# Kernel tuning notes

Hardware: AMD Instinct MI355X
Metric: run time of the kernel (lower is better)

The kernel has to match this reference:

```python
import jax, jax.numpy as jnp
import numpy as np
from functools import partial

G, N, E = 512, 256, 1024
F_IN, EMB, H, NCLS = 30, 256, 3, 2
NEG_SLOPE = 0.2
K1 = int(np.ceil(0.8 * N))   # 205
K2 = int(np.ceil(0.8 * K1))  # 164
K3 = int(np.ceil(0.8 * K2))  # 132


def _gat(x, src, dst, emask, W, asrc, adst, b):
    # Single-graph GATConv (PyG semantics, eval mode): x [n,f], edges [e] + validity mask.
    # Adds self-loops (PyG default), edge-softmax grouped by destination node.
    n = x.shape[0]
    h = (x @ W.T).reshape(n, H, EMB)                      # [n,H,C]
    a_s = (h * asrc).sum(-1)                              # [n,H]
    a_d = (h * adst).sum(-1)                              # [n,H]
    loops = jnp.arange(n, dtype=src.dtype)
    s = jnp.concatenate([src, loops])
    d = jnp.concatenate([dst, loops])
    m = jnp.concatenate([emask, jnp.ones((n,), bool)])
    logit = jax.nn.leaky_relu(a_s[s] + a_d[d], NEG_SLOPE)  # [e+n,H]
    logit = jnp.where(m[:, None], logit, -1e9)
    mx = jax.ops.segment_max(logit, d, num_segments=n)     # stable softmax per dst
    w = jnp.exp(logit - mx[d]) * m[:, None]
    den = jax.ops.segment_sum(w, d, num_segments=n)
    alpha = w / den[d]
    out = jax.ops.segment_sum(alpha[:, :, None] * h[s], d, num_segments=n)  # [n,H,C]
    return out.reshape(n, H * EMB) + b


def _pool(x, src, dst, emask, p, k):
    # TopKPooling: score = tanh((x.p)/||p||); keep top-k nodes, scale by score,
    # remap edge indices and invalidate edges touching dropped nodes.
    n = x.shape[0]
    score = jnp.tanh((x @ p) / jnp.linalg.norm(p))
    vals, perm = jax.lax.top_k(score, k)
    xn = x[perm] * vals[:, None]
    inv = jnp.full((n,), -1, jnp.int32).at[perm].set(jnp.arange(k, dtype=jnp.int32))
    ns, nd = inv[src], inv[dst]
    nm = emask & (ns >= 0) & (nd >= 0)
    return xn, jnp.maximum(ns, 0), jnp.maximum(nd, 0), nm


_gat_b = jax.vmap(_gat, in_axes=(0, 0, 0, 0, None, None, None, None))


def _pool_b(x, src, dst, m, p, k):
    return jax.vmap(partial(_pool, k=k), in_axes=(0, 0, 0, 0, None))(x, src, dst, m, p)


def _readout(x):
    # global_max_pool || global_mean_pool per graph: [G,n,d] -> [G,2d]
    return jnp.concatenate([x.max(axis=1), x.mean(axis=1)], axis=-1)


def _forward(x, edge_src, edge_dst, params):
    (W1, as1, ad1, b1, ht1w, ht1b, p1,
     W2, as2, ad2, b2, ht2w, ht2b, p2,
     W3, as3, ad3, b3, ht3w, ht3b, p3,
     l1w, l1b, l2w, l2b) = params
    src, dst = edge_src, edge_dst
    m = jnp.ones(src.shape, bool)
    h = _gat_b(x, src, dst, m, W1, as1, ad1, b1) @ ht1w.T + ht1b
    h, src, dst, m = _pool_b(h, src, dst, m, p1, K1)
    x1 = _readout(h)
    h = _gat_b(h, src, dst, m, W2, as2, ad2, b2) @ ht2w.T + ht2b
    h, src, dst, m = _pool_b(h, src, dst, m, p2, K2)
    x2 = _readout(h)
    h = _gat_b(h, src, dst, m, W3, as3, ad3, b3) @ ht3w.T + ht3b
    h, src, dst, m = _pool_b(h, src, dst, m, p3, K3)
    x3 = _readout(h)
    z = x1 + x2 + x3
    z = jax.nn.relu(z @ l1w.T + l1b)  # F.dropout is a no-op in eval mode
    return z @ l2w.T + l2b


def setup_inputs() -> dict:
    key = jax.random.key(0)
    keys = iter(jax.random.split(key, 64))
    def nrm(shape, s=0.05):
        return jax.random.normal(next(keys), shape, jnp.float32) * s
    inp = {
        "x": jax.random.normal(next(keys), (G, N, F_IN), jnp.float32),
        "edge_src": jax.random.randint(next(keys), (G, E), 0, N, jnp.int32),
        "edge_dst": jax.random.randint(next(keys), (G, E), 0, N, jnp.int32),
    }
    for i, fin in ((1, F_IN), (2, EMB), (3, EMB)):
        inp[f"W{i}"] = nrm((H * EMB, fin))
        inp[f"asrc{i}"] = nrm((H, EMB))
        inp[f"adst{i}"] = nrm((H, EMB))
        inp[f"b{i}"] = jnp.zeros((H * EMB,), jnp.float32)
        inp[f"ht{i}_w"] = nrm((EMB, H * EMB))
        inp[f"ht{i}_b"] = jnp.zeros((EMB,), jnp.float32)
        inp[f"p{i}"] = nrm((EMB,), 1.0)
    inp["lin1_w"] = nrm((EMB, 2 * EMB))
    inp["lin1_b"] = jnp.zeros((EMB,), jnp.float32)
    inp["lin2_w"] = nrm((NCLS, EMB))
    inp["lin2_b"] = jnp.zeros((NCLS,), jnp.float32)
    return inp


def reference(x, edge_src, edge_dst,
              W1, asrc1, adst1, b1, ht1_w, ht1_b, p1,
              W2, asrc2, adst2, b2, ht2_w, ht2_b, p2,
              W3, asrc3, adst3, b3, ht3_w, ht3_b, p3,
              lin1_w, lin1_b, lin2_w, lin2_b):
    params = (W1, asrc1, adst1, b1, ht1_w, ht1_b, p1,
              W2, asrc2, adst2, b2, ht2_w, ht2_b, p2,
              W3, asrc3, adst3, b3, ht3_w, ht3_b, p3,
              lin1_w, lin1_b, lin2_w, lin2_b)
    return _forward(x, edge_src, edge_dst, params)
```

## Files before the change

kernel.cpp:

```cpp
#include <hip/hip_runtime.h>
#include <hip/hip_bf16.h>

#define GG 512
#define NMAX 256
#define EE 1024
#define HH 3
#define EMB 256
#define NEDGE 1280
#define NEG 0.2f

typedef __attribute__((ext_vector_type(8))) short bf16x8;
typedef __attribute__((ext_vector_type(4))) float f32x4;
#define MFMA16(A,B,C) __builtin_amdgcn_mfma_f32_16x16x32_bf16((A),(B),(C),0,0,0)

__device__ inline void bsplit(float v, unsigned short& s0, unsigned short& s1,
                              unsigned short& s2) {
  __hip_bfloat16 b0 = __float2bfloat16(v);
  float r1 = v - __bfloat162float(b0);
  __hip_bfloat16 b1 = __float2bfloat16(r1);
  float r2 = r1 - __bfloat162float(b1);
  __hip_bfloat16 b2 = __float2bfloat16(r2);
  s0 = *(unsigned short*)&b0; s1 = *(unsigned short*)&b1; s2 = *(unsigned short*)&b2;
}

__global__ void k_prep_wa(const float* __restrict__ W, const float* __restrict__ asrc,
                          const float* __restrict__ adst, float* __restrict__ wa_s,
                          float* __restrict__ wa_d, int f) {
  int t = blockIdx.x * blockDim.x + threadIdx.x;
  int tot = HH * f;
  if (t >= 2 * tot) return;
  int which = t / tot;
  int r = t - which * tot;
  int hd = r / f, ff = r - hd * f;
  const float* a = which ? adst : asrc;
  float s = 0.f;
  for (int c = 0; c < EMB; ++c)
    s += a[hd * EMB + c] * W[(size_t)(hd * EMB + c) * f + ff];
  (which ? wa_d : wa_s)[r] = s;
}

__global__ void k_prep_mcatP(const float* __restrict__ W, const float* __restrict__ htw,
                             float* __restrict__ mcat, int f, int KP) {
  int t = blockIdx.x * blockDim.x + threadIdx.x;
  if (t >= KP * EMB) return;
  int row = t >> 8, j = t & 255;
  float s = 0.f;
  if (row < 3 * f) {
    int hd = row / f, ff = row - hd * f;
    for (int c = 0; c < EMB; ++c)
      s += htw[(size_t)j * (HH * EMB) + hd * EMB + c] * W[(size_t)(hd * EMB + c) * f + ff];
  }
  mcat[(size_t)row * EMB + j] = s;
}

__global__ void k_prep_bt3(const float* __restrict__ mcat, unsigned short* __restrict__ B0,
                           unsigned short* __restrict__ B1, unsigned short* __restrict__ B2,
                           int KP) {
  int t = blockIdx.x * blockDim.x + threadIdx.x;
  if (t >= 256 * KP) return;
  int n = t / KP, k = t - n * KP;
  float v = mcat[(size_t)k * 256 + n];
  unsigned short s0, s1, s2;
  bsplit(v, s0, s1, s2);
  B0[t] = s0; B1[t] = s1; B2[t] = s2;
}

__global__ void k_prep_bb(const float* __restrict__ b, const float* __restrict__ htw,
                          const float* __restrict__ htb, float* __restrict__ bb) {
  int j = threadIdx.x;
  float s = htb[j];
  for (int k = 0; k < HH * EMB; ++k) s += b[k] * htw[(size_t)j * (HH * EMB) + k];
  bb[j] = s;
}

__global__ void k_prep_q(const float* __restrict__ mcat, const float* __restrict__ p,
                         double* __restrict__ qv, int f) {
  int r = blockIdx.x * blockDim.x + threadIdx.x;
  if (r >= 3 * f) return;
  double s = 0.0;
  for (int c = 0; c < EMB; ++c) s += (double)mcat[(size_t)r * EMB + c] * (double)p[c];
  qv[r] = s;
}

__global__ void k_prep_sc(const float* __restrict__ p, const float* __restrict__ bb,
                          double* __restrict__ sc2) {
  __shared__ double sh[256], sh2[256];
  int t = threadIdx.x;
  double pv = (double)p[t];
  sh[t] = pv * pv;
  sh2[t] = (double)bb[t] * pv;
  __syncthreads();
  for (int s = 128; s > 0; s >>= 1) {
    if (t < s) { sh[t] += sh[t + s]; sh2[t] += sh2[t + s]; }
    __syncthreads();
  }
  if (t == 0) { sc2[0] = sh2[0]; sc2[1] = sqrt(sh[0]); }
}

__global__ void k_initedges(const int* __restrict__ s_in, const int* __restrict__ d_in_,
                            int* __restrict__ es, int* __restrict__ ed,
                            int* __restrict__ em, int gc) {
  int t = blockIdx.x * blockDim.x + threadIdx.x;
  if (t >= gc * EE) return;
  es[t] = s_in[t]; ed[t] = d_in_[t]; em[t] = 1;
}

__global__ __launch_bounds__(256) void k_attn2(
    const float* __restrict__ x, const float* __restrict__ wa_s,
    const float* __restrict__ wa_d, const double* __restrict__ qv,
    float* __restrict__ a_s, float* __restrict__ a_d, double* __restrict__ tdot,
    int gc, int n_in, int f) {
  int t = blockIdx.x * blockDim.x + threadIdx.x;
  if (t >= gc * n_in) return;
  int g = t / n_in, i = t - g * n_in;
  const float* xr = x + ((size_t)g * n_in + i) * f;
  float s0 = 0, s1 = 0, s2 = 0, d0 = 0, d1 = 0, d2 = 0;
  double t0 = 0, t1 = 0, t2 = 0;
  for (int c = 0; c < f; ++c) {
    float xv = xr[c];
    s0 += xv * wa_s[0 * f + c]; s1 += xv * wa_s[1 * f + c]; s2 += xv * wa_s[2 * f + c];
    d0 += xv * wa_d[0 * f + c]; d1 += xv * wa_d[1 * f + c]; d2 += xv * wa_d[2 * f + c];
    double xd = (double)xv;
    t0 += xd * qv[0 * f + c]; t1 += xd * qv[1 * f + c]; t2 += xd * qv[2 * f + c];
  }
  size_t o = ((size_t)g * NMAX + i) * HH;
  a_s[o + 0] = s0; a_s[o + 1] = s1; a_s[o + 2] = s2;
  a_d[o + 0] = d0; a_d[o + 1] = d1; a_d[o + 2] = d2;
  tdot[o + 0] = t0; tdot[o + 1] = t1; tdot[o + 2] = t2;
}

__global__ __launch_bounds__(256) void k_graph(
    int* __restrict__ es, int* __restrict__ ed, int* __restrict__ em,
    const float* __restrict__ a_s, const float* __restrict__ a_d,
    const double* __restrict__ tdot, const double* __restrict__ sc2,
    float4* __restrict__ a4, int* __restrict__ coff, int* __restrict__ elist,
    int* __restrict__ sel, float* __restrict__ val, int n_in, int kout) {
  __shared__ float lgs[NEDGE * 3];
  __shared__ unsigned short sdst[NEDGE], ssrc[NEDGE];
  __shared__ unsigned char sval[NEDGE];
  __shared__ int cnt2[256];
  __shared__ int off[257];
  __shared__ int elist_s[NEDGE];
  __shared__ float sscore[256];
  __shared__ unsigned long long keys[256];
  __shared__ int inv[256];
  int g = blockIdx.x, tid = threadIdx.x;
  int etot = EE + n_in;
  cnt2[tid] = 0;
  __syncthreads();
  for (int e = tid; e < etot; e += 256) {
    int s, d, v;
    if (e < EE) { s = es[g * EE + e]; d = ed[g * EE + e]; v = em[g * EE + e]; }
    else { s = d = e - EE; v = 1; }
    sdst[e] = (unsigned short)d; ssrc[e] = (unsigned short)s; sval[e] = (unsigned char)v;
    if (v) {
      const float* as = a_s + ((size_t)g * NMAX + s) * HH;
      const float* ad = a_d + ((size_t)g * NMAX + d) * HH;
#pragma unroll
      for (int h = 0; h < HH; ++h) {
        float lv = as[h] + ad[h];
        lgs[e * 3 + h] = lv > 0.f ? lv : NEG * lv;
      }
      atomicAdd(&cnt2[d], 1);
    }
  }
  __syncthreads();
  if (tid == 0) {
    int run = 0;
    for (int i = 0; i < n_in; ++i) { int c = cnt2[i]; off[i] = run; run += c; }
    off[n_in] = run;
  }
  __syncthreads();
  for (int i = tid; i <= n_in; i += 256) coff[g * 257 + i] = off[i];
  cnt2[tid] = 0;
  __syncthreads();
  for (int e = tid; e < etot; e += 256) {
    if (sval[e]) {
      int d = sdst[e];
      int pos = atomicAdd(&cnt2[d], 1);
      elist_s[off[d] + pos] = e;
    }
  }
  __syncthreads();
  if (tid < n_in) {
    int o0 = off[tid], o1 = off[tid + 1];
    for (int i = o0 + 1; i < o1; ++i) {
      int key = elist_s[i];
      int j = i - 1;
      while (j >= o0 && elist_s[j] > key) { elist_s[j + 1] = elist_s[j]; --j; }
      elist_s[j + 1] = key;
    }
    for (int q = o0; q < o1; ++q) elist[g * NEDGE + q] = elist_s[q];
  }
  __syncthreads();
  float sc = -3e38f;
  if (tid < n_in) {
    int o0 = off[tid], o1 = off[tid + 1];
    float m0 = -1e30f, m1 = -1e30f, m2 = -1e30f;
    for (int q = o0; q < o1; ++q) {
      int e = elist_s[q];
      m0 = fmaxf(m0, lgs[e * 3 + 0]);
      m1 = fmaxf(m1, lgs[e * 3 + 1]);
      m2 = fmaxf(m2, lgs[e * 3 + 2]);
    }
    float d0 = 0, d1 = 0, d2 = 0;
    for (int q = o0; q < o1; ++q) {
      int e = elist_s[q];
      d0 += expf(lgs[e * 3 + 0] - m0);
      d1 += expf(lgs[e * 3 + 1] - m1);
      d2 += expf(lgs[e * 3 + 2] - m2);
    }
    float r0 = 1.f / d0, r1 = 1.f / d1, r2 = 1.f / d2;
    double s = 0.0;
    for (int q = o0; q < o1; ++q) {
      int e = elist_s[q];
      float w0 = expf(lgs[e * 3 + 0] - m0) * r0;
      float w1 = expf(lgs[e * 3 + 1] - m1) * r1;
      float w2 = expf(lgs[e * 3 + 2] - m2) * r2;
      int src = ssrc[e];
      float4 av; av.x = w0; av.y = w1; av.z = w2; av.w = __int_as_float(src);
      a4[(size_t)g * NEDGE + e] = av;
      const double* td = tdot + ((size_t)g * NMAX + src) * HH;
      s += (double)w0 * td[0] + (double)w1 * td[1] + (double)w2 * td[2];
    }
    sc = (float)tanh((s + sc2[0]) / sc2[1]);
  }
  sscore[tid] = sc;
  unsigned int u = __float_as_uint(sc);
  unsigned int ord = (u & 0x80000000u) ? ~u : (u | 0x80000000u);
  unsigned long long key = ((unsigned long long)(~ord) << 32) | (unsigned int)tid;
  if (tid >= n_in) key = 0xFFFFFFFF00000000ull | (unsigned int)tid;
  keys[tid] = key;
  __syncthreads();
  for (int kk = 2; kk <= 256; kk <<= 1) {
    for (int j = kk >> 1; j > 0; j >>= 1) {
      int ixj = tid ^ j;
      if (ixj > tid) {
        unsigned long long a = keys[tid], b = keys[ixj];
        bool up = ((tid & kk) == 0);
        if (up ? (a > b) : (a < b)) { keys[tid] = b; keys[ixj] = a; }
      }
      __syncthreads();
    }
  }
  inv[tid] = -1;
  __syncthreads();
  if (tid < kout) {
    int pi = (int)(keys[tid] & 0xFFFFu);
    inv[pi] = tid;
    sel[g * 256 + tid] = pi;
    val[g * 256 + tid] = sscore[pi];
  }
  __syncthreads();
  for (int e = tid; e < EE; e += 256) {
    int s = es[g * EE + e], d = ed[g * EE + e], m = em[g * EE + e];
    int ns = inv[s], nd = inv[d];
    int nm = (m && ns >= 0 && nd >= 0) ? 1 : 0;
    es[g * EE + e] = ns < 0 ? 0 : ns;
    ed[g * EE + e] = nd < 0 ? 0 : nd;
    em[g * EE + e] = nm;
  }
}

template<bool F256>
__global__ __launch_bounds__(256) void k_gather_sel(
    const float* __restrict__ xin, const float4* __restrict__ a4,
    const int* __restrict__ coff, const int* __restrict__ elist,
    const int* __restrict__ sel,
    unsigned short* __restrict__ A0, unsigned short* __restrict__ A1,
    unsigned short* __restrict__ A2,
    int gc, int n_in, int n_out, int f, int KP) {
  int wid = (blockIdx.x * blockDim.x + threadIdx.x) >> 6;
  int lane = threadIdx.x & 63;
  if (wid >= gc * n_out) return;
  int g = wid / n_out, j = wid - g * n_out;
  int pi = sel[(g << 8) + j];
  int o0 = coff[g * 257 + pi], o1 = coff[g * 257 + pi + 1];
  const float* xg = xin + (size_t)g * n_in * f;
  size_t rb = ((size_t)g * n_out + j) * (size_t)KP;
  if (F256) {
    float4 acc0 = make_float4(0, 0, 0, 0);
    float4 acc1 = make_float4(0, 0, 0, 0);
    float4 acc2 = make_float4(0, 0, 0, 0);
    for (int t = o0; t < o1; ++t) {
      int e = elist[g * NEDGE + t];
      float4 a = a4[(size_t)g * NEDGE + e];
      int src = __float_as_int(a.w);
      float4 xv = ((const float4*)(xg + (size_t)src * 256))[lane];
      acc0.x += a.x * xv.x; acc0.y += a.x * xv.y; acc0.z += a.x * xv.z; acc0.w += a.x * xv.w;
      acc1.x += a.y * xv.x; acc1.y += a.y * xv.y; acc1.z += a.y * xv.z; acc1.w += a.y * xv.w;
      acc2.x += a.z * xv.x; acc2.y += a.z * xv.y; acc2.z += a.z * xv.z; acc2.w += a.z * xv.w;
    }
    float4 accs[3] = {acc0, acc1, acc2};
#pragma unroll
    for (int h = 0; h < 3; ++h) {
      size_t idx = rb + (size_t)h * 256 + lane * 4;
      ushort4 u0, u1, u2;
      bsplit(accs[h].x, u0.x, u1.x, u2.x);
      bsplit(accs[h].y, u0.y, u1.y, u2.y);
      bsplit(accs[h].z, u0.z, u1.z, u2.z);
      bsplit(accs[h].w, u0.w, u1.w, u2.w);
      *(ushort4*)&A0[idx] = u0;
      *(ushort4*)&A1[idx] = u1;
      *(ushort4*)&A2[idx] = u2;
    }
  } else {
    for (int kk = lane; kk < 96; kk += 64) {
      float v = 0.f;
      if (kk < 90) {
        int h = kk / 30, cc = kk - h * 30;
        for (int t = o0; t < o1; ++t) {
          int e = elist[g * NEDGE + t];
          float4 a = a4[(size_t)g * NEDGE + e];
          int src = __float_as_int(a.w);
          float al = (h == 0) ? a.x : ((h == 1) ? a.y : a.z);
          v += al * xg[(size_t)src * 30 + cc];
        }
      }
      unsigned short s0, s1, s2;
      bsplit(v, s0, s1, s2);
      A0[rb + kk] = s0; A1[rb + kk] = s1; A2[rb + kk] = s2;
    }
  }
}

__global__ __launch_bounds__(256) void k_mgemm(
    const unsigned short* __restrict__ A0, const unsigned short* __restrict__ A1,
    const unsigned short* __restrict__ A2,
    const unsigned short* __restrict__ B0, const unsigned short* __restrict__ B1,
    const unsigned short* __restrict__ B2,
    const float* __restrict__ bias, const float* __restrict__ val,
    float* __restrict__ xout, int Mrows, int KP, int n_out, int nbx) {
  __shared__ unsigned short As[3][64 * 32];
  __shared__ unsigned short Bs[3][64 * 32];
  int tid = threadIdx.x;
  int jj = blockIdx.x & 31;
  int rr0 = (blockIdx.x >> 5) * 8 + (jj & 7);
  int cc0 = jj >> 3;
  if (rr0 >= nbx) return;
  int row0 = rr0 * 64;
  int col0 = cc0 * 64;
  int lane = tid & 63, w = tid >> 6;
  int kg = lane >> 4, r16 = lane & 15;
  int wr = (w >> 1) * 32, wc = (w & 1) * 32;
  int sr = tid >> 2, sj = tid & 3;
  int sp = sj ^ ((sr >> 1) & 3);
  const unsigned short* Ap[3] = {A0, A1, A2};
  const unsigned short* Bp[3] = {B0, B1, B2};

  f32x4 acc[2][2];
#pragma unroll
  for (int i = 0; i < 2; ++i)
#pragma unroll
    for (int j = 0; j < 2; ++j) acc[i][j] = (f32x4){0.f, 0.f, 0.f, 0.f};

  int nkt = KP >> 5;
  for (int kt = 0; kt < nkt; ++kt) {
    int k0 = kt << 5;
    int gra = row0 + sr;
    int grb = col0 + sr;
#pragma unroll
    for (int p = 0; p < 3; ++p) {
      uint4 va = make_uint4(0, 0, 0, 0);
      if (gra < Mrows) va = *(const uint4*)&Ap[p][(size_t)gra * KP + k0 + (sj << 3)];
      *(uint4*)&As[p][sr * 32 + (sp << 3)] = va;
      uint4 vb = *(const uint4*)&Bp[p][(size_t)grb * KP + k0 + (sj << 3)];
      *(uint4*)&Bs[p][sr * 32 + (sp << 3)] = vb;
    }
    __syncthreads();
    bf16x8 af[2][3], bf[2][3];
#pragma unroll
    for (int fm = 0; fm < 2; ++fm) {
      int row = wr + (fm << 4) + r16;
      int pk = kg ^ ((row >> 1) & 3);
#pragma unroll
      for (int p = 0; p < 3; ++p)
        af[fm][p] = *(const bf16x8*)&As[p][row * 32 + (pk << 3)];
    }
#pragma unroll
    for (int fn = 0; fn < 2; ++fn) {
      int col = wc + (fn << 4) + r16;
      int pk = kg ^ ((col >> 1) & 3);
#pragma unroll
      for (int p = 0; p < 3; ++p)
        bf[fn][p] = *(const bf16x8*)&Bs[p][col * 32 + (pk << 3)];
    }
#pragma unroll
    for (int fm = 0; fm < 2; ++fm)
#pragma unroll
      for (int fn = 0; fn < 2; ++fn) {
        f32x4 c = acc[fm][fn];
        c = MFMA16(af[fm][0], bf[fn][0], c);
        c = MFMA16(af[fm][0], bf[fn][1], c);
        c = MFMA16(af[fm][1], bf[fn][0], c);
        c = MFMA16(af[fm][0], bf[fn][2], c);
        c = MFMA16(af[fm][2], bf[fn][0], c);
        c = MFMA16(af[fm][1], bf[fn][1], c);
        acc[fm][fn] = c;
      }
    __syncthreads();
  }
#pragma unroll
  for (int fm = 0; fm < 2; ++fm)
#pragma unroll
    for (int fn = 0; fn < 2; ++fn) {
      int colg = col0 + wc + (fn << 4) + r16;
      float bi = bias[colg];
#pragma unroll
      for (int rr = 0; rr < 4; ++rr) {
        int rowg = row0 + wr + (fm << 4) + (kg << 2) + rr;
        if (rowg < Mrows) {
          int gg = rowg / n_out, j = rowg - gg * n_out;
          xout[((size_t)gg * n_out + j) * EMB + colg] =
              (acc[fm][fn][rr] + bi) * val[(gg << 8) + j];
        }
      }
    }
}

__global__ void k_readout(const float* __restrict__ x, float* __restrict__ z,
                          int n_out, int g0) {
  int g = blockIdx.x, c = threadIdx.x;
  float mx = -3e38f, sm = 0.f;
  for (int j = 0; j < n_out; ++j) {
    float v = x[((size_t)g * n_out + j) * EMB + c];
    mx = fmaxf(mx, v);
    sm += v;
  }
  z[(size_t)(g0 + g) * 512 + c] += mx;
  z[(size_t)(g0 + g) * 512 + 256 + c] += sm / (float)n_out;
}

__global__ void k_mlp(const float* __restrict__ z, const float* __restrict__ l1w,
                      const float* __restrict__ l1b, const float* __restrict__ l2w,
                      const float* __restrict__ l2b, float* __restrict__ out) {
  __shared__ float zs[512];
  __shared__ float h1[256];
  int g = blockIdx.x, tid = threadIdx.x;
  zs[tid] = z[(size_t)g * 512 + tid];
  zs[256 + tid] = z[(size_t)g * 512 + 256 + tid];
  __syncthreads();
  float s = l1b[tid];
  for (int c = 0; c < 512; ++c) s += zs[c] * l1w[(size_t)tid * 512 + c];
  h1[tid] = s > 0.f ? s : 0.f;
  __syncthreads();
  if (tid < 2) {
    float o = l2b[tid];
    for (int c = 0; c < 256; ++c) o += h1[c] * l2w[(size_t)tid * 256 + c];
    out[g * 2 + tid] = o;
  }
}

extern "C" void kernel_launch(void* const* d_in, const int* in_sizes, int n_in_cnt,
                              void* d_out, int out_size, void* d_ws, size_t ws_size,
                              hipStream_t stream) {
  (void)in_sizes; (void)n_in_cnt; (void)out_size;
  const float* x0 = (const float*)d_in[0];
  const int* e_src = (const int*)d_in[1];
  const int* e_dst = (const int*)d_in[2];
  struct LP { const float *W, *as, *ad, *b, *hw, *hb, *p; int f, nin, nout, KP; };
  LP L[3];
  for (int l = 0; l < 3; ++l) {
    int base = 3 + l * 7;
    L[l].W  = (const float*)d_in[base + 0];
    L[l].as = (const float*)d_in[base + 1];
    L[l].ad = (const float*)d_in[base + 2];
    L[l].b  = (const float*)d_in[base + 3];
    L[l].hw = (const float*)d_in[base + 4];
    L[l].hb = (const float*)d_in[base + 5];
    L[l].p  = (const float*)d_in[base + 6];
  }
  L[0].f = 30;  L[1].f = 256; L[2].f = 256;
  L[0].nin = 256; L[0].nout = 205; L[0].KP = 96;
  L[1].nin = 205; L[1].nout = 164; L[1].KP = 768;
  L[2].nin = 164; L[2].nout = 132; L[2].KP = 768;
  const float* l1w = (const float*)d_in[24];
  const float* l1b = (const float*)d_in[25];
  const float* l2w = (const float*)d_in[26];
  const float* l2b = (const float*)d_in[27];
  float* out = (float*)d_out;

  char* w = (char*)d_ws;
  char* wend = w + ws_size;
  auto alloc = [&](size_t bytes) {
    char* r = w; w += (bytes + 255) & ~(size_t)255; return r;
  };
  float*  z = (float*)alloc((size_t)GG * 512 * 4);
  float *wa_s[3], *wa_d[3], *mcatP[3], *bbv[3];
  unsigned short *bt0[3], *bt1[3], *bt2[3];
  double *qv[3], *sc2[3];
  for (int l = 0; l < 3; ++l) {
    int KP = (l == 0) ? 96 : 768;
    wa_s[l]  = (float*)alloc((size_t)HH * 256 * 4);
    wa_d[l]  = (float*)alloc((size_t)HH * 256 * 4);
    mcatP[l] = (float*)alloc((size_t)768 * EMB * 4);
    bbv[l]   = (float*)alloc((size_t)EMB * 4);
    bt0[l]   = (unsigned short*)alloc((size_t)256 * KP * 2);
    bt1[l]   = (unsigned short*)alloc((size_t)256 * KP * 2);
    bt2[l]   = (unsigned short*)alloc((size_t)256 * KP * 2);
    qv[l]    = (double*)alloc((size_t)768 * 8);
    sc2[l]   = (double*)alloc(256);
  }

  const size_t AMAX = (size_t)164 * 768;
  const size_t APAD = (size_t)64 * 768;
  size_t fixed_used = (size_t)(w - (char*)d_ws);
  size_t per_g = (size_t)205 * EMB * 4
               + AMAX * 2 * 3
               + (size_t)NMAX * HH * 4 * 2
               + (size_t)NMAX * HH * 8
               + (size_t)NEDGE * 16
               + (size_t)EE * 4 * 3
               + (size_t)257 * 4 + (size_t)NEDGE * 4
               + (size_t)256 * 4 * 2
               + 24 * 256;
  size_t avail = (ws_size > fixed_used + 1048576) ? (ws_size - fixed_used - 1048576) : 0;
  int Gc = (int)(avail / per_g);
  if (Gc > GG) Gc = GG;
  if (Gc < 1) Gc = 1;
  int nchunks = (GG + Gc - 1) / Gc;
  Gc = (GG + nchunks - 1) / nchunks;

  float*  xbuf = (float*)alloc((size_t)Gc * 205 * EMB * 4);
  unsigned short* AP0 = (unsigned short*)alloc(((size_t)Gc * AMAX + APAD) * 2);
  unsigned short* AP1 = (unsigned short*)alloc(((size_t)Gc * AMAX + APAD) * 2);
  unsigned short* AP2 = (unsigned short*)alloc(((size_t)Gc * AMAX + APAD) * 2);
  float*  a_s  = (float*)alloc((size_t)Gc * NMAX * HH * 4);
  float*  a_d  = (float*)alloc((size_t)Gc * NMAX * HH * 4);
  double* tdot = (double*)alloc((size_t)Gc * NMAX * HH * 8);
  float4* a4   = (float4*)alloc((size_t)Gc * NEDGE * 16);
  int*    es   = (int*)alloc((size_t)Gc * EE * 4);
  int*    ed   = (int*)alloc((size_t)Gc * EE * 4);
  int*    em   = (int*)alloc((size_t)Gc * EE * 4);
  int*    coff = (int*)alloc((size_t)Gc * 257 * 4);
  int*    elist= (int*)alloc((size_t)Gc * NEDGE * 4);
  int*    sel  = (int*)alloc((size_t)Gc * 256 * 4);
  float*  val  = (float*)alloc((size_t)Gc * 256 * 4);
  if (w > wend) return;

  (void)hipMemsetAsync(z, 0, (size_t)GG * 512 * 4, stream);

  for (int l = 0; l < 3; ++l) {
    int f = L[l].f, KP = L[l].KP;
    k_prep_wa<<<(2 * HH * f + 255) / 256, 256, 0, stream>>>(L[l].W, L[l].as, L[l].ad, wa_s[l], wa_d[l], f);
    k_prep_mcatP<<<(KP * EMB + 255) / 256, 256, 0, stream>>>(L[l].W, L[l].hw, mcatP[l], f, KP);
    k_prep_bt3<<<(256 * KP + 255) / 256, 256, 0, stream>>>(mcatP[l], bt0[l], bt1[l], bt2[l], KP);
    k_prep_bb<<<1, 256, 0, stream>>>(L[l].b, L[l].hw, L[l].hb, bbv[l]);
    k_prep_q<<<(3 * f + 255) / 256, 256, 0, stream>>>(mcatP[l], L[l].p, qv[l], f);
    k_prep_sc<<<1, 256, 0, stream>>>(L[l].p, bbv[l], sc2[l]);
  }

  for (int g0 = 0; g0 < GG; g0 += Gc) {
    int gc = (GG - g0 < Gc) ? (GG - g0) : Gc;
    { int tot = gc * EE;
      k_initedges<<<(tot + 255) / 256, 256, 0, stream>>>(
          e_src + (size_t)g0 * EE, e_dst + (size_t)g0 * EE, es, ed, em, gc); }
    const float* xin = x0 + (size_t)g0 * 256 * 30;
    for (int l = 0; l < 3; ++l) {
      int f = L[l].f, nin = L[l].nin, nout = L[l].nout, KP = L[l].KP;
      k_attn2<<<(gc * nin + 255) / 256, 256, 0, stream>>>(xin, wa_s[l], wa_d[l], qv[l], a_s, a_d, tdot, gc, nin, f);
      k_graph<<<gc, 256, 0, stream>>>(es, ed, em, a_s, a_d, tdot, sc2[l], a4, coff, elist, sel, val, nin, nout);
      { int waves = gc * nout;
        if (f == 256)
          k_gather_sel<true><<<(waves * 64 + 255) / 256, 256, 0, stream>>>(
              xin, a4, coff, elist, sel, AP0, AP1, AP2, gc, nin, nout, f, KP);
        else
          k_gather_sel<false><<<(waves * 64 + 255) / 256, 256, 0, stream>>>(
              xin, a4, coff, elist, sel, AP0, AP1, AP2, gc, nin, nout, f, KP);
      }
      { int Mrows = gc * nout;
        int nbx = (Mrows + 63) / 64;
        int nblk = ((nbx + 7) / 8) * 32;
        k_mgemm<<<nblk, 256, 0, stream>>>(AP0, AP1, AP2, bt0[l], bt1[l], bt2[l],
                                          bbv[l], val, xbuf, Mrows, KP, nout, nbx);
      }
      k_readout<<<gc, 256, 0, stream>>>(xbuf, z, nout, g0);
      xin = xbuf;
    }
  }
  k_mlp<<<GG, 256, 0, stream>>>(z, l1w, l1b, l2w, l2b, out);
}
```

Measured before the change: 2.163 ms.

## Double-buffer GEMM LDS tiles and fold edge init into graph kernel

The split-bf16 MFMA GEMM now double-buffers its A/B shared-memory tiles. The next K-tile's global loads are issued into registers before computing the current tile, which removes one barrier per iteration and overlaps memory latency with MFMA work. Launch bounds ask for 3 blocks per SM, and doubling the LDS footprint may limit occupancy. Separately, the edge-init kernel is removed: the first layer's graph kernel reads the input edges directly, and edge remapping reuses the indices already cached in shared memory instead of reloading them from global.

```diff
diff --git a/kernel.cpp b/kernel.cpp
--- a/kernel.cpp
+++ b/kernel.cpp
@@ -95,14 +95,6 @@
     __syncthreads();
   }
   if (t == 0) { sc2[0] = sh2[0]; sc2[1] = sqrt(sh[0]); }
-}
-
-__global__ void k_initedges(const int* __restrict__ s_in, const int* __restrict__ d_in_,
-                            int* __restrict__ es, int* __restrict__ ed,
-                            int* __restrict__ em, int gc) {
-  int t = blockIdx.x * blockDim.x + threadIdx.x;
-  if (t >= gc * EE) return;
-  es[t] = s_in[t]; ed[t] = d_in_[t]; em[t] = 1;
 }
 
 __global__ __launch_bounds__(256) void k_attn2(
@@ -130,6 +122,7 @@
 }
 
 __global__ __launch_bounds__(256) void k_graph(
+    const int* __restrict__ src_in, const int* __restrict__ dst_in, int first,
     int* __restrict__ es, int* __restrict__ ed, int* __restrict__ em,
     const float* __restrict__ a_s, const float* __restrict__ a_d,
     const double* __restrict__ tdot, const double* __restrict__ sc2,
@@ -150,8 +143,10 @@
   __syncthreads();
   for (int e = tid; e < etot; e += 256) {
     int s, d, v;
-    if (e < EE) { s = es[g * EE + e]; d = ed[g * EE + e]; v = em[g * EE + e]; }
-    else { s = d = e - EE; v = 1; }
+    if (e < EE) {
+      if (first) { s = src_in[g * EE + e]; d = dst_in[g * EE + e]; v = 1; }
+      else { s = es[g * EE + e]; d = ed[g * EE + e]; v = em[g * EE + e]; }
+    } else { s = d = e - EE; v = 1; }
     sdst[e] = (unsigned short)d; ssrc[e] = (unsigned short)s; sval[e] = (unsigned char)v;
     if (v) {
       const float* as = a_s + ((size_t)g * NMAX + s) * HH;
@@ -253,7 +248,7 @@
   }
   __syncthreads();
   for (int e = tid; e < EE; e += 256) {
-    int s = es[g * EE + e], d = ed[g * EE + e], m = em[g * EE + e];
+    int s = ssrc[e], d = sdst[e], m = sval[e];
     int ns = inv[s], nd = inv[d];
     int nm = (m && ns >= 0 && nd >= 0) ? 1 : 0;
     es[g * EE + e] = ns < 0 ? 0 : ns;
@@ -324,15 +319,15 @@
   }
 }
 
-__global__ __launch_bounds__(256) void k_mgemm(
+__global__ __launch_bounds__(256, 3) void k_mgemm(
     const unsigned short* __restrict__ A0, const unsigned short* __restrict__ A1,
     const unsigned short* __restrict__ A2,
     const unsigned short* __restrict__ B0, const unsigned short* __restrict__ B1,
     const unsigned short* __restrict__ B2,
     const float* __restrict__ bias, const float* __restrict__ val,
     float* __restrict__ xout, int Mrows, int KP, int n_out, int nbx) {
-  __shared__ unsigned short As[3][64 * 32];
-  __shared__ unsigned short Bs[3][64 * 32];
+  __shared__ unsigned short As[2][3][64 * 32];
+  __shared__ unsigned short Bs[2][3][64 * 32];
   int tid = threadIdx.x;
   int jj = blockIdx.x & 31;
   int rr0 = (blockIdx.x >> 5) * 8 + (jj & 7);
@@ -354,20 +349,30 @@
 #pragma unroll
     for (int j = 0; j < 2; ++j) acc[i][j] = (f32x4){0.f, 0.f, 0.f, 0.f};
 
-  int nkt = KP >> 5;
-  for (int kt = 0; kt < nkt; ++kt) {
+  uint4 ra0, ra1, ra2, rb0, rb1, rb2;
+  auto gload = [&](int kt) {
     int k0 = kt << 5;
-    int gra = row0 + sr;
-    int grb = col0 + sr;
-#pragma unroll
-    for (int p = 0; p < 3; ++p) {
-      uint4 va = make_uint4(0, 0, 0, 0);
-      if (gra < Mrows) va = *(const uint4*)&Ap[p][(size_t)gra * KP + k0 + (sj << 3)];
-      *(uint4*)&As[p][sr * 32 + (sp << 3)] = va;
-      uint4 vb = *(const uint4*)&Bp[p][(size_t)grb * KP + k0 + (sj << 3)];
-      *(uint4*)&Bs[p][sr * 32 + (sp << 3)] = vb;
-    }
-    __syncthreads();
+    int gra = row0 + sr, grb = col0 + sr;
+    ra0 = make_uint4(0, 0, 0, 0); ra1 = ra0; ra2 = ra0;
+    if (gra < Mrows) {
+      ra0 = *(const uint4*)&Ap[0][(size_t)gra * KP + k0 + (sj << 3)];
+      ra1 = *(const uint4*)&Ap[1][(size_t)gra * KP + k0 + (sj << 3)];
+      ra2 = *(const uint4*)&Ap[2][(size_t)gra * KP + k0 + (sj << 3)];
+    }
+    rb0 = *(const uint4*)&Bp[0][(size_t)grb * KP + k0 + (sj << 3)];
+    rb1 = *(const uint4*)&Bp[1][(size_t)grb * KP + k0 + (sj << 3)];
+    rb2 = *(const uint4*)&Bp[2][(size_t)grb * KP + k0 + (sj << 3)];
+  };
+  auto lwrite = [&](int b) {
+    int o = sr * 32 + (sp << 3);
+    *(uint4*)&As[b][0][o] = ra0;
+    *(uint4*)&As[b][1][o] = ra1;
+    *(uint4*)&As[b][2][o] = ra2;
+    *(uint4*)&Bs[b][0][o] = rb0;
+    *(uint4*)&Bs[b][1][o] = rb1;
+    *(uint4*)&Bs[b][2][o] = rb2;
+  };
+  auto compute = [&](int b) {
     bf16x8 af[2][3], bf[2][3];
 #pragma unroll
     for (int fm = 0; fm < 2; ++fm) {
@@ -375,7 +380,7 @@
       int pk = kg ^ ((row >> 1) & 3);
 #pragma unroll
       for (int p = 0; p < 3; ++p)
-        af[fm][p] = *(const bf16x8*)&As[p][row * 32 + (pk << 3)];
+        af[fm][p] = *(const bf16x8*)&As[b][p][row * 32 + (pk << 3)];
     }
 #pragma unroll
     for (int fn = 0; fn < 2; ++fn) {
@@ -383,7 +388,7 @@
       int pk = kg ^ ((col >> 1) & 3);
 #pragma unroll
       for (int p = 0; p < 3; ++p)
-        bf[fn][p] = *(const bf16x8*)&Bs[p][col * 32 + (pk << 3)];
+        bf[fn][p] = *(const bf16x8*)&Bs[b][p][col * 32 + (pk << 3)];
     }
 #pragma unroll
     for (int fm = 0; fm < 2; ++fm)
@@ -398,6 +403,17 @@
         c = MFMA16(af[fm][1], bf[fn][1], c);
         acc[fm][fn] = c;
       }
+  };
+
+  int nkt = KP >> 5;
+  gload(0);
+  lwrite(0);
+  __syncthreads();
+  for (int kt = 0; kt < nkt; ++kt) {
+    int b = kt & 1;
+    if (kt + 1 < nkt) gload(kt + 1);
+    compute(b);
+    if (kt + 1 < nkt) lwrite(b ^ 1);
     __syncthreads();
   }
 #pragma unroll
@@ -552,14 +568,13 @@
 
   for (int g0 = 0; g0 < GG; g0 += Gc) {
     int gc = (GG - g0 < Gc) ? (GG - g0) : Gc;
-    { int tot = gc * EE;
-      k_initedges<<<(tot + 255) / 256, 256, 0, stream>>>(
-          e_src + (size_t)g0 * EE, e_dst + (size_t)g0 * EE, es, ed, em, gc); }
     const float* xin = x0 + (size_t)g0 * 256 * 30;
     for (int l = 0; l < 3; ++l) {
       int f = L[l].f, nin = L[l].nin, nout = L[l].nout, KP = L[l].KP;
       k_attn2<<<(gc * nin + 255) / 256, 256, 0, stream>>>(xin, wa_s[l], wa_d[l], qv[l], a_s, a_d, tdot, gc, nin, f);
-      k_graph<<<gc, 256, 0, stream>>>(es, ed, em, a_s, a_d, tdot, sc2[l], a4, coff, elist, sel, val, nin, nout);
+      k_graph<<<gc, 256, 0, stream>>>(e_src + (size_t)g0 * EE, e_dst + (size_t)g0 * EE,
+                                      (l == 0) ? 1 : 0, es, ed, em,
+                                      a_s, a_d, tdot, sc2[l], a4, coff, elist, sel, val, nin, nout);
       { int waves = gc * nout;
         if (f == 256)
           k_gather_sel<true><<<(waves * 64 + 255) / 256, 256, 0, stream>>>(
```

Measured after the change: 2.146 ms. About the same (-0.8%).

## Fuse attention-score and edge init into graph kernel; widen GEMM tile to 128 columns

Applied to the files above, without the earlier changes.

Folds the per-node attention and score dot products (formerly k_attn2) into k_graph, keeping them in shared memory instead of global buffers. It also reads the raw edge inputs directly on the first layer, which removes the k_initedges launch. The GEMM tile grows from 64x64 to 64x128 per block with a 3-blocks-per-SM launch bound, raising reuse of the A tile. The trade-off is that the fused per-node dot products now run only 256 threads per graph, which may be slow for f=256 since each thread loops over 256 features serially. The GEMM change adds register pressure.

```diff
diff --git a/kernel.cpp b/kernel.cpp
--- a/kernel.cpp
+++ b/kernel.cpp
@@ -97,47 +97,19 @@
   if (t == 0) { sc2[0] = sh2[0]; sc2[1] = sqrt(sh[0]); }
 }
 
-__global__ void k_initedges(const int* __restrict__ s_in, const int* __restrict__ d_in_,
-                            int* __restrict__ es, int* __restrict__ ed,
-                            int* __restrict__ em, int gc) {
-  int t = blockIdx.x * blockDim.x + threadIdx.x;
-  if (t >= gc * EE) return;
-  es[t] = s_in[t]; ed[t] = d_in_[t]; em[t] = 1;
-}
-
-__global__ __launch_bounds__(256) void k_attn2(
-    const float* __restrict__ x, const float* __restrict__ wa_s,
+__global__ __launch_bounds__(256) void k_graph(
+    const int* __restrict__ src_in, const int* __restrict__ dst_in, int first,
+    int* __restrict__ es, int* __restrict__ ed, int* __restrict__ em,
+    const float* __restrict__ xin, const float* __restrict__ wa_s,
     const float* __restrict__ wa_d, const double* __restrict__ qv,
-    float* __restrict__ a_s, float* __restrict__ a_d, double* __restrict__ tdot,
-    int gc, int n_in, int f) {
-  int t = blockIdx.x * blockDim.x + threadIdx.x;
-  if (t >= gc * n_in) return;
-  int g = t / n_in, i = t - g * n_in;
-  const float* xr = x + ((size_t)g * n_in + i) * f;
-  float s0 = 0, s1 = 0, s2 = 0, d0 = 0, d1 = 0, d2 = 0;
-  double t0 = 0, t1 = 0, t2 = 0;
-  for (int c = 0; c < f; ++c) {
-    float xv = xr[c];
-    s0 += xv * wa_s[0 * f + c]; s1 += xv * wa_s[1 * f + c]; s2 += xv * wa_s[2 * f + c];
-    d0 += xv * wa_d[0 * f + c]; d1 += xv * wa_d[1 * f + c]; d2 += xv * wa_d[2 * f + c];
-    double xd = (double)xv;
-    t0 += xd * qv[0 * f + c]; t1 += xd * qv[1 * f + c]; t2 += xd * qv[2 * f + c];
-  }
-  size_t o = ((size_t)g * NMAX + i) * HH;
-  a_s[o + 0] = s0; a_s[o + 1] = s1; a_s[o + 2] = s2;
-  a_d[o + 0] = d0; a_d[o + 1] = d1; a_d[o + 2] = d2;
-  tdot[o + 0] = t0; tdot[o + 1] = t1; tdot[o + 2] = t2;
-}
-
-__global__ __launch_bounds__(256) void k_graph(
-    int* __restrict__ es, int* __restrict__ ed, int* __restrict__ em,
-    const float* __restrict__ a_s, const float* __restrict__ a_d,
-    const double* __restrict__ tdot, const double* __restrict__ sc2,
+    const double* __restrict__ sc2,
     float4* __restrict__ a4, int* __restrict__ coff, int* __restrict__ elist,
-    int* __restrict__ sel, float* __restrict__ val, int n_in, int kout) {
+    int* __restrict__ sel, float* __restrict__ val, int n_in, int f, int kout) {
   __shared__ float lgs[NEDGE * 3];
   __shared__ unsigned short sdst[NEDGE], ssrc[NEDGE];
   __shared__ unsigned char sval[NEDGE];
+  __shared__ float sas[256][3], sad[256][3];
+  __shared__ double stdt[256][3];
   __shared__ int cnt2[256];
   __shared__ int off[257];
   __shared__ int elist_s[NEDGE];
@@ -147,18 +119,33 @@
   int g = blockIdx.x, tid = threadIdx.x;
   int etot = EE + n_in;
   cnt2[tid] = 0;
+  if (tid < n_in) {
+    const float* xr = xin + ((size_t)g * n_in + tid) * f;
+    float s0 = 0, s1 = 0, s2 = 0, d0 = 0, d1 = 0, d2 = 0;
+    double t0 = 0, t1 = 0, t2 = 0;
+    for (int c = 0; c < f; ++c) {
+      float xv = xr[c];
+      s0 += xv * wa_s[c]; s1 += xv * wa_s[f + c]; s2 += xv * wa_s[2 * f + c];
+      d0 += xv * wa_d[c]; d1 += xv * wa_d[f + c]; d2 += xv * wa_d[2 * f + c];
+      double xd = (double)xv;
+      t0 += xd * qv[c]; t1 += xd * qv[f + c]; t2 += xd * qv[2 * f + c];
+    }
+    sas[tid][0] = s0; sas[tid][1] = s1; sas[tid][2] = s2;
+    sad[tid][0] = d0; sad[tid][1] = d1; sad[tid][2] = d2;
+    stdt[tid][0] = t0; stdt[tid][1] = t1; stdt[tid][2] = t2;
+  }
   __syncthreads();
   for (int e = tid; e < etot; e += 256) {
     int s, d, v;
-    if (e < EE) { s = es[g * EE + e]; d = ed[g * EE + e]; v = em[g * EE + e]; }
-    else { s = d = e - EE; v = 1; }
+    if (e < EE) {
+      if (first) { s = src_in[g * EE + e]; d = dst_in[g * EE + e]; v = 1; }
+      else { s = es[g * EE + e]; d = ed[g * EE + e]; v = em[g * EE + e]; }
+    } else { s = d = e - EE; v = 1; }
     sdst[e] = (unsigned short)d; ssrc[e] = (unsigned short)s; sval[e] = (unsigned char)v;
     if (v) {
-      const float* as = a_s + ((size_t)g * NMAX + s) * HH;
-      const float* ad = a_d + ((size_t)g * NMAX + d) * HH;
 #pragma unroll
       for (int h = 0; h < HH; ++h) {
-        float lv = as[h] + ad[h];
+        float lv = sas[s][h] + sad[d][h];
         lgs[e * 3 + h] = lv > 0.f ? lv : NEG * lv;
       }
       atomicAdd(&cnt2[d], 1);
@@ -220,8 +207,7 @@
       int src = ssrc[e];
       float4 av; av.x = w0; av.y = w1; av.z = w2; av.w = __int_as_float(src);
       a4[(size_t)g * NEDGE + e] = av;
-      const double* td = tdot + ((size_t)g * NMAX + src) * HH;
-      s += (double)w0 * td[0] + (double)w1 * td[1] + (double)w2 * td[2];
+      s += (double)w0 * stdt[src][0] + (double)w1 * stdt[src][1] + (double)w2 * stdt[src][2];
     }
     sc = (float)tanh((s + sc2[0]) / sc2[1]);
   }
@@ -253,7 +239,7 @@
   }
   __syncthreads();
   for (int e = tid; e < EE; e += 256) {
-    int s = es[g * EE + e], d = ed[g * EE + e], m = em[g * EE + e];
+    int s = ssrc[e], d = sdst[e], m = sval[e];
     int ns = inv[s], nd = inv[d];
     int nm = (m && ns >= 0 && nd >= 0) ? 1 : 0;
     es[g * EE + e] = ns < 0 ? 0 : ns;
@@ -324,7 +310,7 @@
   }
 }
 
-__global__ __launch_bounds__(256) void k_mgemm(
+__global__ __launch_bounds__(256, 3) void k_mgemm(
     const unsigned short* __restrict__ A0, const unsigned short* __restrict__ A1,
     const unsigned short* __restrict__ A2,
     const unsigned short* __restrict__ B0, const unsigned short* __restrict__ B1,
@@ -332,43 +318,53 @@
     const float* __restrict__ bias, const float* __restrict__ val,
     float* __restrict__ xout, int Mrows, int KP, int n_out, int nbx) {
   __shared__ unsigned short As[3][64 * 32];
-  __shared__ unsigned short Bs[3][64 * 32];
+  __shared__ unsigned short Bs[3][128 * 32];
   int tid = threadIdx.x;
-  int jj = blockIdx.x & 31;
-  int rr0 = (blockIdx.x >> 5) * 8 + (jj & 7);
-  int cc0 = jj >> 3;
+  int jj = blockIdx.x & 15;
+  int rr0 = (blockIdx.x >> 4) * 8 + (jj & 7);
+  int cc0 = (jj >> 3) & 1;
   if (rr0 >= nbx) return;
   int row0 = rr0 * 64;
-  int col0 = cc0 * 64;
+  int col0 = cc0 * 128;
   int lane = tid & 63, w = tid >> 6;
   int kg = lane >> 4, r16 = lane & 15;
-  int wr = (w >> 1) * 32, wc = (w & 1) * 32;
+  int wr = (w >> 1) * 32, wc = (w & 1) * 64;
   int sr = tid >> 2, sj = tid & 3;
-  int sp = sj ^ ((sr >> 1) & 3);
+  int spA = sj ^ ((sr >> 1) & 3);
   const unsigned short* Ap[3] = {A0, A1, A2};
   const unsigned short* Bp[3] = {B0, B1, B2};
 
-  f32x4 acc[2][2];
+  f32x4 acc[2][4];
 #pragma unroll
   for (int i = 0; i < 2; ++i)
 #pragma unroll
-    for (int j = 0; j < 2; ++j) acc[i][j] = (f32x4){0.f, 0.f, 0.f, 0.f};
+    for (int j = 0; j < 4; ++j) acc[i][j] = (f32x4){0.f, 0.f, 0.f, 0.f};
 
   int nkt = KP >> 5;
   for (int kt = 0; kt < nkt; ++kt) {
     int k0 = kt << 5;
-    int gra = row0 + sr;
-    int grb = col0 + sr;
-#pragma unroll
-    for (int p = 0; p < 3; ++p) {
-      uint4 va = make_uint4(0, 0, 0, 0);
-      if (gra < Mrows) va = *(const uint4*)&Ap[p][(size_t)gra * KP + k0 + (sj << 3)];
-      *(uint4*)&As[p][sr * 32 + (sp << 3)] = va;
-      uint4 vb = *(const uint4*)&Bp[p][(size_t)grb * KP + k0 + (sj << 3)];
-      *(uint4*)&Bs[p][sr * 32 + (sp << 3)] = vb;
+    {
+      int gra = row0 + sr;
+#pragma unroll
+      for (int p = 0; p < 3; ++p) {
+        uint4 va = make_uint4(0, 0, 0, 0);
+        if (gra < Mrows) va = *(const uint4*)&Ap[p][(size_t)gra * KP + k0 + (sj << 3)];
+        *(uint4*)&As[p][sr * 32 + (spA << 3)] = va;
+      }
+    }
+#pragma unroll
+    for (int s = 0; s < 2; ++s) {
+      int c = tid + (s << 8);
+      int col = c >> 2, cg = c & 3;
+      int sp = cg ^ ((col >> 1) & 3);
+#pragma unroll
+      for (int p = 0; p < 3; ++p) {
+        uint4 vb = *(const uint4*)&Bp[p][(size_t)(col0 + col) * KP + k0 + (cg << 3)];
+        *(uint4*)&Bs[p][col * 32 + (sp << 3)] = vb;
+      }
     }
     __syncthreads();
-    bf16x8 af[2][3], bf[2][3];
+    bf16x8 af[2][3], bf[4][3];
 #pragma unroll
     for (int fm = 0; fm < 2; ++fm) {
       int row = wr + (fm << 4) + r16;
@@ -378,7 +374,7 @@
         af[fm][p] = *(const bf16x8*)&As[p][row * 32 + (pk << 3)];
     }
 #pragma unroll
-    for (int fn = 0; fn < 2; ++fn) {
+    for (int fn = 0; fn < 4; ++fn) {
       int col = wc + (fn << 4) + r16;
       int pk = kg ^ ((col >> 1) & 3);
 #pragma unroll
@@ -386,9 +382,9 @@
         bf[fn][p] = *(const bf16x8*)&Bs[p][col * 32 + (pk << 3)];
     }
 #pragma unroll
-    for (int fm = 0; fm < 2; ++fm)
-#pragma unroll
-      for (int fn = 0; fn < 2; ++fn) {
+    for (int fn = 0; fn < 4; ++fn)
+#pragma unroll
+      for (int fm = 0; fm < 2; ++fm) {
         f32x4 c = acc[fm][fn];
         c = MFMA16(af[fm][0], bf[fn][0], c);
         c = MFMA16(af[fm][0], bf[fn][1], c);
@@ -403,7 +399,7 @@
 #pragma unroll
   for (int fm = 0; fm < 2; ++fm)
 #pragma unroll
-    for (int fn = 0; fn < 2; ++fn) {
+    for (int fn = 0; fn < 4; ++fn) {
       int colg = col0 + wc + (fn << 4) + r16;
       float bi = bias[colg];
 #pragma unroll
@@ -507,8 +503,6 @@
   size_t fixed_used = (size_t)(w - (char*)d_ws);
   size_t per_g = (size_t)205 * EMB * 4
                + AMAX * 2 * 3
-               + (size_t)NMAX * HH * 4 * 2
-               + (size_t)NMAX * HH * 8
                + (size_t)NEDGE * 16
                + (size_t)EE * 4 * 3
                + (size_t)257 * 4 + (size_t)NEDGE * 4
@@ -525,9 +519,6 @@
   unsigned short* AP0 = (unsigned short*)alloc(((size_t)Gc * AMAX + APAD) * 2);
   unsigned short* AP1 = (unsigned short*)alloc(((size_t)Gc * AMAX + APAD) * 2);
   unsigned short* AP2 = (unsigned short*)alloc(((size_t)Gc * AMAX + APAD) * 2);
-  float*  a_s  = (float*)alloc((size_t)Gc * NMAX * HH * 4);
-  float*  a_d  = (float*)alloc((size_t)Gc * NMAX * HH * 4);
-  double* tdot = (double*)alloc((size_t)Gc * NMAX * HH * 8);
   float4* a4   = (float4*)alloc((size_t)Gc * NEDGE * 16);
   int*    es   = (int*)alloc((size_t)Gc * EE * 4);
   int*    ed   = (int*)alloc((size_t)Gc * EE * 4);
@@ -552,14 +543,13 @@
 
   for (int g0 = 0; g0 < GG; g0 += Gc) {
     int gc = (GG - g0 < Gc) ? (GG - g0) : Gc;
-    { int tot = gc * EE;
-      k_initedges<<<(tot + 255) / 256, 256, 0, stream>>>(
-          e_src + (size_t)g0 * EE, e_dst + (size_t)g0 * EE, es, ed, em, gc); }
     const float* xin = x0 + (size_t)g0 * 256 * 30;
     for (int l = 0; l < 3; ++l) {
       int f = L[l].f, nin = L[l].nin, nout = L[l].nout, KP = L[l].KP;
-      k_attn2<<<(gc * nin + 255) / 256, 256, 0, stream>>>(xin, wa_s[l], wa_d[l], qv[l], a_s, a_d, tdot, gc, nin, f);
-      k_graph<<<gc, 256, 0, stream>>>(es, ed, em, a_s, a_d, tdot, sc2[l], a4, coff, elist, sel, val, nin, nout);
+      k_graph<<<gc, 256, 0, stream>>>(e_src + (size_t)g0 * EE, e_dst + (size_t)g0 * EE,
+                                      (l == 0) ? 1 : 0, es, ed, em,
+                                      xin, wa_s[l], wa_d[l], qv[l], sc2[l],
+                                      a4, coff, elist, sel, val, nin, f, nout);
       { int waves = gc * nout;
         if (f == 256)
           k_gather_sel<true><<<(waves * 64 + 255) / 256, 256, 0, stream>>>(
@@ -570,7 +560,7 @@
       }
       { int Mrows = gc * nout;
         int nbx = (Mrows + 63) / 64;
-        int nblk = ((nbx + 7) / 8) * 32;
+        int nblk = ((nbx + 7) / 8) * 16;
         k_mgemm<<<nblk, 256, 0, stream>>>(AP0, AP1, AP2, bt0[l], bt1[l], bt2[l],
                                           bbv[l], val, xbuf, Mrows, KP, nout, nbx);
       }
```

After: 1.827 ms. -15.5%, faster.
